# Kernel optimization log

Measured on AMD Instinct MI355X. Metric: run time of the kernel, lower is better.

Reference implementation:

```python
import jax, jax.numpy as jnp
import numpy as np

D_MODEL = 1024
N_HEADS = 16
D_K = D_MODEL // N_HEADS


def setup_inputs() -> dict:
    key = jax.random.key(0)
    ks = jax.random.split(key, 7)
    s = 1.0 / np.sqrt(D_MODEL)
    return {
        "x": jax.random.normal(ks[0], (2, 2048, D_MODEL), dtype=jnp.float32),
        "w_q": jax.random.uniform(ks[1], (D_MODEL, D_MODEL), jnp.float32, -s, s),
        "w_k": jax.random.uniform(ks[2], (D_MODEL, D_MODEL), jnp.float32, -s, s),
        "w_v": jax.random.uniform(ks[3], (D_MODEL, D_MODEL), jnp.float32, -s, s),
        "w_o": jax.random.uniform(ks[4], (D_MODEL, D_MODEL), jnp.float32, -s, s),
        "b_o": jax.random.uniform(ks[5], (D_MODEL,), jnp.float32, -s, s),
        "ln_gamma": jnp.ones((D_MODEL,), jnp.float32),
        "ln_beta": jnp.zeros((D_MODEL,), jnp.float32),
    }


def reference(x, w_q, w_k, w_v, w_o, b_o, ln_gamma, ln_beta):
    # Pre-LN
    mu = jnp.mean(x, axis=-1, keepdims=True)
    var = jnp.mean(jnp.square(x - mu), axis=-1, keepdims=True)
    x_norm = (x - mu) / jnp.sqrt(var + 1e-5) * ln_gamma + ln_beta

    B, S, _ = x.shape
    # torch Linear: y = x @ W.T ; weights stored [out, in]
    def proj(w):
        return (x_norm @ w.T).reshape(B, S, N_HEADS, D_K).transpose(0, 2, 1, 3)

    Q, K, V = proj(w_q), proj(w_k), proj(w_v)  # [B,H,S,Dk]
    scores = jnp.einsum("bhqd,bhkd->bhqk", Q, K) / np.sqrt(D_K)
    attn = jax.nn.softmax(scores, axis=-1)
    attended = jnp.einsum("bhqk,bhkd->bhqd", attn, V)
    attended = attended.transpose(0, 2, 1, 3).reshape(B, S, D_MODEL)
    out = attended @ w_o.T + b_o
    return x + out
```

## Files before the change

### kernel.cpp

```cpp
#include <hip/hip_runtime.h>

typedef _Float16 f16;
typedef _Float16 f16x8 __attribute__((ext_vector_type(8)));
typedef _Float16 f16x4 __attribute__((ext_vector_type(4)));
typedef float f32x4 __attribute__((ext_vector_type(4)));

#define SEQ   2048
#define DM    1024
#define DKH   64
#define MTOT  4096

__device__ __forceinline__ f32x4 mfma16(f16x8 a, f16x8 b, f32x4 c) {
  return __builtin_amdgcn_mfma_f32_16x16x32_f16(a, b, c, 0, 0, 0);
}

__device__ __forceinline__ void gload16(const f16* g, f16* l) {
  __builtin_amdgcn_global_load_lds(
      (const __attribute__((address_space(1))) void*)g,
      (__attribute__((address_space(3))) void*)l, 16, 0, 0);
}

__global__ __launch_bounds__(256) void cast_all(const float* __restrict__ w_q,
                                                const float* __restrict__ w_k,
                                                const float* __restrict__ w_v,
                                                const float* __restrict__ w_o,
                                                f16* __restrict__ out) {
  const int sel = blockIdx.x >> 10;
  const float* src = sel == 0 ? w_q : sel == 1 ? w_k : sel == 2 ? w_v : w_o;
  const int i = ((blockIdx.x & 1023) * 256 + threadIdx.x) * 4;
  float4 v = *reinterpret_cast<const float4*>(src + i);
  f16x4 o;
  o[0] = (f16)v.x; o[1] = (f16)v.y; o[2] = (f16)v.z; o[3] = (f16)v.w;
  *reinterpret_cast<f16x4*>(out + (size_t)sel * 1048576 + i) = o;
}

__global__ __launch_bounds__(256) void ln_kernel(const float* __restrict__ x,
                                                 const float* __restrict__ gamma,
                                                 const float* __restrict__ beta,
                                                 f16* __restrict__ xn) {
  const int row = blockIdx.x, t = threadIdx.x;
  const float* xr = x + (size_t)row * DM;
  float v[4], s = 0.f, s2 = 0.f;
#pragma unroll
  for (int i = 0; i < 4; ++i) {
    v[i] = xr[t + i * 256];
    s += v[i];
    s2 += v[i] * v[i];
  }
#pragma unroll
  for (int o = 32; o > 0; o >>= 1) {
    s  += __shfl_down(s, o);
    s2 += __shfl_down(s2, o);
  }
  __shared__ float ps[4], ps2[4], mu_s, rs_s;
  if ((t & 63) == 0) { ps[t >> 6] = s; ps2[t >> 6] = s2; }
  __syncthreads();
  if (t == 0) {
    float a = ps[0] + ps[1] + ps[2] + ps[3];
    float b = ps2[0] + ps2[1] + ps2[2] + ps2[3];
    float mu = a * (1.f / DM);
    float var = b * (1.f / DM) - mu * mu;
    mu_s = mu;
    rs_s = rsqrtf(var + 1e-5f);
  }
  __syncthreads();
  const float mu = mu_s, rs = rs_s;
#pragma unroll
  for (int i = 0; i < 4; ++i) {
    int d = t + i * 256;
    xn[(size_t)row * DM + d] = (f16)(((v[i] - mu) * rs) * gamma[d] + beta[d]);
  }
}

__global__ __launch_bounds__(256) void gemm_qkv(const f16* __restrict__ A,
                                                const f16* __restrict__ Wqkv,
                                                f16* __restrict__ qb,
                                                f16* __restrict__ kb,
                                                f16* __restrict__ vtb) {
  __shared__ f16 sA[128][64];
  __shared__ f16 sB[64][64];
  const int t = threadIdx.x, l = t & 63, w = t >> 6;
  const int wr = w >> 1, wc = w & 1, lg = l >> 4, lm = l & 15;
  const int m0 = blockIdx.y * 128, n0 = blockIdx.x * 64;
  const int crow = l >> 3;
  const int scol = ((l & 7) ^ crow) << 3;
  const int rsw  = (lm & 7) << 3;

  f32x4 acc[4][2] = {};

  for (int k0 = 0; k0 < DM; k0 += 64) {
    __syncthreads();
#pragma unroll
    for (int cc = 0; cc < 4; ++cc) {
      const int c = w + cc * 4;
      gload16(A + (size_t)(m0 + c * 8 + crow) * DM + k0 + scol, &sA[c * 8][0]);
    }
#pragma unroll
    for (int cc = 0; cc < 2; ++cc) {
      const int c = w + cc * 4;
      gload16(Wqkv + (size_t)(n0 + c * 8 + crow) * DM + k0 + scol, &sB[c * 8][0]);
    }
    __syncthreads();
#pragma unroll
    for (int kk = 0; kk < 2; ++kk) {
      f16x8 af[4], bf[2];
#pragma unroll
      for (int i = 0; i < 4; ++i)
        af[i] = *(const f16x8*)&sA[wr * 64 + i * 16 + lm][(kk * 32 + lg * 8) ^ rsw];
#pragma unroll
      for (int i = 0; i < 2; ++i)
        bf[i] = *(const f16x8*)&sB[wc * 32 + i * 16 + lm][(kk * 32 + lg * 8) ^ rsw];
#pragma unroll
      for (int mi = 0; mi < 4; ++mi)
#pragma unroll
        for (int ni = 0; ni < 2; ++ni)
          acc[mi][ni] = mfma16(af[mi], bf[ni], acc[mi][ni]);
    }
  }

  const int sel = blockIdx.x >> 4;
  if (sel < 2) {
    f16* outp = sel == 0 ? qb : kb;
    const int nloc = n0 - sel * 1024;
#pragma unroll
    for (int mi = 0; mi < 4; ++mi) {
      const int rowb = m0 + wr * 64 + mi * 16 + lg * 4;
#pragma unroll
      for (int ni = 0; ni < 2; ++ni) {
        const int col = nloc + wc * 32 + ni * 16 + lm;
#pragma unroll
        for (int r = 0; r < 4; ++r)
          outp[(size_t)(rowb + r) * DM + col] = (f16)acc[mi][ni][r];
      }
    }
  } else {
#pragma unroll
    for (int mi = 0; mi < 4; ++mi) {
      const int rowb = m0 + wr * 64 + mi * 16 + lg * 4;
      const int b = rowb >> 11, s = rowb & 2047;
#pragma unroll
      for (int ni = 0; ni < 2; ++ni) {
        const int col = (n0 - 2048) + wc * 32 + ni * 16 + lm;
        f16x4 o;
        o[0] = (f16)acc[mi][ni][0]; o[1] = (f16)acc[mi][ni][1];
        o[2] = (f16)acc[mi][ni][2]; o[3] = (f16)acc[mi][ni][3];
        *reinterpret_cast<f16x4*>(&vtb[(size_t)(b * 1024 + col) * SEQ + s]) = o;
      }
    }
  }
}

__global__ __launch_bounds__(256) void gemm_out(const f16* __restrict__ A,
                                                const f16* __restrict__ W,
                                                float* __restrict__ out,
                                                const float* __restrict__ bias,
                                                const float* __restrict__ resid) {
  __shared__ f16 sA[64][64];
  __shared__ f16 sB[128][64];
  const int t = threadIdx.x, l = t & 63, w = t >> 6;
  const int wr = w >> 1, wc = w & 1, lg = l >> 4, lm = l & 15;
  const int m0 = blockIdx.y * 64, n0 = blockIdx.x * 128;
  const int crow = l >> 3;
  const int scol = ((l & 7) ^ crow) << 3;
  const int rsw  = (lm & 7) << 3;

  f32x4 acc[2][4] = {};

  for (int k0 = 0; k0 < DM; k0 += 64) {
    __syncthreads();
#pragma unroll
    for (int cc = 0; cc < 2; ++cc) {
      const int c = w + cc * 4;
      gload16(A + (size_t)(m0 + c * 8 + crow) * DM + k0 + scol, &sA[c * 8][0]);
    }
#pragma unroll
    for (int cc = 0; cc < 4; ++cc) {
      const int c = w + cc * 4;
      gload16(W + (size_t)(n0 + c * 8 + crow) * DM + k0 + scol, &sB[c * 8][0]);
    }
    __syncthreads();
#pragma unroll
    for (int kk = 0; kk < 2; ++kk) {
      f16x8 af[2], bf[4];
#pragma unroll
      for (int i = 0; i < 2; ++i)
        af[i] = *(const f16x8*)&sA[wr * 32 + i * 16 + lm][(kk * 32 + lg * 8) ^ rsw];
#pragma unroll
      for (int i = 0; i < 4; ++i)
        bf[i] = *(const f16x8*)&sB[wc * 64 + i * 16 + lm][(kk * 32 + lg * 8) ^ rsw];
#pragma unroll
      for (int mi = 0; mi < 2; ++mi)
#pragma unroll
        for (int ni = 0; ni < 4; ++ni)
          acc[mi][ni] = mfma16(af[mi], bf[ni], acc[mi][ni]);
    }
  }

#pragma unroll
  for (int mi = 0; mi < 2; ++mi) {
    const int rowb = m0 + wr * 32 + mi * 16 + lg * 4;
#pragma unroll
    for (int ni = 0; ni < 4; ++ni) {
      const int col = n0 + wc * 64 + ni * 16 + lm;
#pragma unroll
      for (int r = 0; r < 4; ++r) {
        const size_t idx = (size_t)(rowb + r) * DM + col;
        out[idx] = resid[idx] + bias[col] + acc[mi][ni][r];
      }
    }
  }
}

__global__ __launch_bounds__(256) void attn_kernel(const f16* __restrict__ Qb,
                                                   const f16* __restrict__ Kb,
                                                   const f16* __restrict__ Vt,
                                                   f16* __restrict__ Ob) {
  __shared__ f16 sK[2][64][64];
  __shared__ f16 sV[2][64][64];

  int bx = blockIdx.x;
  bx = (bx & 7) * 128 + (bx >> 3);
  const int qt = bx & 31, bh = bx >> 5;
  const int h = bh & 15, b = bh >> 4;
  const int t = threadIdx.x, l = t & 63, w = t >> 6;
  const int lg = l >> 4, lm = l & 15;
  const float K2 = 0.18033688f;

  const f16* qptr = Qb + (size_t)(b * SEQ + qt * 64 + w * 16 + lm) * DM + h * DKH;
  f16x8 qf[2];
  qf[0] = *(const f16x8*)(qptr + lg * 8);
  qf[1] = *(const f16x8*)(qptr + 32 + lg * 8);
#pragma unroll
  for (int j = 0; j < 8; ++j) {
    qf[0][j] = (f16)((float)qf[0][j] * K2);
    qf[1][j] = (f16)((float)qf[1][j] * K2);
  }

  float lsum = 0.f;
  f32x4 oacc[4] = {};

  const int crow = l >> 3;
  const int scol = ((l & 7) ^ crow) << 3;
  const int rsw  = (lm & 7) << 3;

  auto stage = [&](int buf, int kt) {
#pragma unroll
    for (int cc = 0; cc < 2; ++cc) {
      const int c = w + cc * 4;
      const int row = c * 8 + crow;
      const int nfp = row >> 4, lgp = (row >> 2) & 3, rp = row & 3;
      const int key = (nfp >> 1) * 32 + lgp * 8 + (nfp & 1) * 4 + rp;
      gload16(Kb + (size_t)(b * SEQ + kt * 64 + key) * DM + h * DKH + scol,
              &sK[buf][c * 8][0]);
      gload16(Vt + (size_t)(bh * DKH + row) * SEQ + kt * 64 + scol,
              &sV[buf][c * 8][0]);
    }
  };

  stage(0, 0);
  __syncthreads();
  int cur = 0;

  for (int kt = 0; kt < SEQ / 64; ++kt) {
    if (kt < SEQ / 64 - 1) stage(cur ^ 1, kt + 1);

    f32x4 sc[4] = {};
    __builtin_amdgcn_s_setprio(1);
#pragma unroll
    for (int kk = 0; kk < 2; ++kk)
#pragma unroll
      for (int nf = 0; nf < 4; ++nf) {
        f16x8 kf = *(const f16x8*)&sK[cur][nf * 16 + lm][(kk * 32 + lg * 8) ^ rsw];
        sc[nf] = mfma16(kf, qf[kk], sc[nf]);
      }
    __builtin_amdgcn_s_setprio(0);

    f16x8 pf[2];
#pragma unroll
    for (int nf = 0; nf < 4; ++nf)
#pragma unroll
      for (int r = 0; r < 4; ++r) {
        float p = __builtin_amdgcn_exp2f(sc[nf][r]);
        lsum += p;
        pf[nf >> 1][(nf & 1) * 4 + r] = (f16)p;
      }

    __builtin_amdgcn_s_setprio(1);
#pragma unroll
    for (int ks = 0; ks < 2; ++ks)
#pragma unroll
      for (int ni = 0; ni < 4; ++ni) {
        f16x8 vf = *(const f16x8*)&sV[cur][ni * 16 + lm][(ks * 32 + lg * 8) ^ rsw];
        oacc[ni] = mfma16(pf[ks], vf, oacc[ni]);
      }
    __builtin_amdgcn_s_setprio(0);

    __syncthreads();
    cur ^= 1;
  }

  float denom = lsum;
  denom += __shfl_xor(denom, 16);
  denom += __shfl_xor(denom, 32);
  float rd[4];
#pragma unroll
  for (int r = 0; r < 4; ++r) rd[r] = 1.f / __shfl(denom, lg * 4 + r);

#pragma unroll
  for (int ni = 0; ni < 4; ++ni)
#pragma unroll
    for (int r = 0; r < 4; ++r) {
      const int q = qt * 64 + w * 16 + lg * 4 + r;
      const int d = ni * 16 + lm;
      Ob[(size_t)(b * SEQ + q) * DM + h * DKH + d] = (f16)(oacc[ni][r] * rd[r]);
    }
}

extern "C" void kernel_launch(void* const* d_in, const int* in_sizes, int n_in,
                              void* d_out, int out_size, void* d_ws, size_t ws_size,
                              hipStream_t stream) {
  const float* x   = (const float*)d_in[0];
  const float* w_q = (const float*)d_in[1];
  const float* w_k = (const float*)d_in[2];
  const float* w_v = (const float*)d_in[3];
  const float* w_o = (const float*)d_in[4];
  const float* b_o = (const float*)d_in[5];
  const float* lng = (const float*)d_in[6];
  const float* lnb = (const float*)d_in[7];
  float* out = (float*)d_out;

  char* ws = (char*)d_ws;
  const size_t MB = 1ull << 20;
  f16* xn   = (f16*)(ws + 0 * MB);
  f16* wqkv = (f16*)(ws + 8 * MB);
  f16* woh  = (f16*)(ws + 14 * MB);
  f16* qb   = (f16*)(ws + 16 * MB);
  f16* kb   = (f16*)(ws + 24 * MB);
  f16* vtb  = (f16*)(ws + 32 * MB);
  f16* att  = (f16*)(ws + 40 * MB);

  cast_all<<<4096, 256, 0, stream>>>(w_q, w_k, w_v, w_o, wqkv);
  ln_kernel<<<MTOT, 256, 0, stream>>>(x, lng, lnb, xn);

  gemm_qkv<<<dim3(48, 32), 256, 0, stream>>>(xn, wqkv, qb, kb, vtb);
  attn_kernel<<<1024, 256, 0, stream>>>(qb, kb, vtb, att);
  gemm_out<<<dim3(8, 64), 256, 0, stream>>>(att, woh, out, b_o, x);
}
```

Baseline: 127.7 us.

## Double query rows per attention block and compute denominators via MFMA

Each attention workgroup now handles 128 query rows (32 per wave) instead of 64, so every K/V tile staged into LDS is reused by twice as many MFMAs and half as many blocks are launched. The softmax denominator is now accumulated with an extra MFMA against a ones vector instead of scalar adds plus cross-lane shuffles, and probabilities are packed with cvt_pkrtz. The costs are higher register pressure, fewer blocks (512) to fill the GPU, and round-toward-zero fp16 conversion of the probabilities.

Measured after the change: 121.3 us. 5.0% less time.

```diff
diff --git a/kernel.cpp b/kernel.cpp
--- a/kernel.cpp
+++ b/kernel.cpp
@@ -3,6 +3,8 @@
 typedef _Float16 f16;
 typedef _Float16 f16x8 __attribute__((ext_vector_type(8)));
 typedef _Float16 f16x4 __attribute__((ext_vector_type(4)));
+typedef _Float16 f16x2 __attribute__((ext_vector_type(2)));
+typedef __fp16 fp16x2 __attribute__((ext_vector_type(2)));
 typedef float f32x4 __attribute__((ext_vector_type(4)));
 
 #define SEQ   2048
@@ -12,6 +14,11 @@
 
 __device__ __forceinline__ f32x4 mfma16(f16x8 a, f16x8 b, f32x4 c) {
   return __builtin_amdgcn_mfma_f32_16x16x32_f16(a, b, c, 0, 0, 0);
+}
+
+__device__ __forceinline__ f16x2 cvt_pk(float a, float b) {
+  fp16x2 r = __builtin_amdgcn_cvt_pkrtz(a, b);
+  return __builtin_bit_cast(f16x2, r);
 }
 
 __device__ __forceinline__ void gload16(const f16* g, f16* l) {
@@ -219,25 +226,32 @@
   __shared__ f16 sV[2][64][64];
 
   int bx = blockIdx.x;
-  bx = (bx & 7) * 128 + (bx >> 3);
-  const int qt = bx & 31, bh = bx >> 5;
+  bx = (bx & 7) * 64 + (bx >> 3);
+  const int qt = bx & 15, bh = bx >> 4;
   const int h = bh & 15, b = bh >> 4;
   const int t = threadIdx.x, l = t & 63, w = t >> 6;
   const int lg = l >> 4, lm = l & 15;
   const float K2 = 0.18033688f;
 
-  const f16* qptr = Qb + (size_t)(b * SEQ + qt * 64 + w * 16 + lm) * DM + h * DKH;
-  f16x8 qf[2];
-  qf[0] = *(const f16x8*)(qptr + lg * 8);
-  qf[1] = *(const f16x8*)(qptr + 32 + lg * 8);
-#pragma unroll
-  for (int j = 0; j < 8; ++j) {
-    qf[0][j] = (f16)((float)qf[0][j] * K2);
-    qf[1][j] = (f16)((float)qf[1][j] * K2);
-  }
-
-  float lsum = 0.f;
-  f32x4 oacc[4] = {};
+  f16x8 qf[2][2];
+#pragma unroll
+  for (int qg = 0; qg < 2; ++qg) {
+    const f16* qptr =
+        Qb + (size_t)(b * SEQ + qt * 128 + w * 32 + qg * 16 + lm) * DM + h * DKH;
+    qf[qg][0] = *(const f16x8*)(qptr + lg * 8);
+    qf[qg][1] = *(const f16x8*)(qptr + 32 + lg * 8);
+#pragma unroll
+    for (int j = 0; j < 8; ++j) {
+      qf[qg][0][j] = (f16)((float)qf[qg][0][j] * K2);
+      qf[qg][1][j] = (f16)((float)qf[qg][1][j] * K2);
+    }
+  }
+
+  const f16x8 ones = {(f16)1, (f16)1, (f16)1, (f16)1,
+                      (f16)1, (f16)1, (f16)1, (f16)1};
+
+  f32x4 oacc[2][4] = {};
+  f32x4 oden[2] = {};
 
   const int crow = l >> 3;
   const int scol = ((l & 7) ^ crow) << 3;
@@ -264,56 +278,64 @@
   for (int kt = 0; kt < SEQ / 64; ++kt) {
     if (kt < SEQ / 64 - 1) stage(cur ^ 1, kt + 1);
 
-    f32x4 sc[4] = {};
+    f32x4 sc[2][4] = {};
     __builtin_amdgcn_s_setprio(1);
 #pragma unroll
     for (int kk = 0; kk < 2; ++kk)
 #pragma unroll
       for (int nf = 0; nf < 4; ++nf) {
         f16x8 kf = *(const f16x8*)&sK[cur][nf * 16 + lm][(kk * 32 + lg * 8) ^ rsw];
-        sc[nf] = mfma16(kf, qf[kk], sc[nf]);
+        sc[0][nf] = mfma16(kf, qf[0][kk], sc[0][nf]);
+        sc[1][nf] = mfma16(kf, qf[1][kk], sc[1][nf]);
       }
     __builtin_amdgcn_s_setprio(0);
 
-    f16x8 pf[2];
-#pragma unroll
-    for (int nf = 0; nf < 4; ++nf)
-#pragma unroll
-      for (int r = 0; r < 4; ++r) {
-        float p = __builtin_amdgcn_exp2f(sc[nf][r]);
-        lsum += p;
-        pf[nf >> 1][(nf & 1) * 4 + r] = (f16)p;
+    union PU { f16x8 v; f16x2 h[4]; };
+    PU pu[2][2];
+#pragma unroll
+    for (int qg = 0; qg < 2; ++qg)
+#pragma unroll
+      for (int nf = 0; nf < 4; ++nf) {
+        float e0 = __builtin_amdgcn_exp2f(sc[qg][nf][0]);
+        float e1 = __builtin_amdgcn_exp2f(sc[qg][nf][1]);
+        float e2 = __builtin_amdgcn_exp2f(sc[qg][nf][2]);
+        float e3 = __builtin_amdgcn_exp2f(sc[qg][nf][3]);
+        pu[qg][nf >> 1].h[(nf & 1) * 2 + 0] = cvt_pk(e0, e1);
+        pu[qg][nf >> 1].h[(nf & 1) * 2 + 1] = cvt_pk(e2, e3);
       }
 
     __builtin_amdgcn_s_setprio(1);
 #pragma unroll
-    for (int ks = 0; ks < 2; ++ks)
+    for (int ks = 0; ks < 2; ++ks) {
 #pragma unroll
       for (int ni = 0; ni < 4; ++ni) {
         f16x8 vf = *(const f16x8*)&sV[cur][ni * 16 + lm][(ks * 32 + lg * 8) ^ rsw];
-        oacc[ni] = mfma16(pf[ks], vf, oacc[ni]);
-      }
+        oacc[0][ni] = mfma16(pu[0][ks].v, vf, oacc[0][ni]);
+        oacc[1][ni] = mfma16(pu[1][ks].v, vf, oacc[1][ni]);
+      }
+      oden[0] = mfma16(pu[0][ks].v, ones, oden[0]);
+      oden[1] = mfma16(pu[1][ks].v, ones, oden[1]);
+    }
     __builtin_amdgcn_s_setprio(0);
 
     __syncthreads();
     cur ^= 1;
   }
 
-  float denom = lsum;
-  denom += __shfl_xor(denom, 16);
-  denom += __shfl_xor(denom, 32);
-  float rd[4];
-#pragma unroll
-  for (int r = 0; r < 4; ++r) rd[r] = 1.f / __shfl(denom, lg * 4 + r);
-
-#pragma unroll
-  for (int ni = 0; ni < 4; ++ni)
-#pragma unroll
-    for (int r = 0; r < 4; ++r) {
-      const int q = qt * 64 + w * 16 + lg * 4 + r;
-      const int d = ni * 16 + lm;
-      Ob[(size_t)(b * SEQ + q) * DM + h * DKH + d] = (f16)(oacc[ni][r] * rd[r]);
-    }
+#pragma unroll
+  for (int qg = 0; qg < 2; ++qg) {
+    float rd[4];
+#pragma unroll
+    for (int r = 0; r < 4; ++r) rd[r] = 1.f / oden[qg][r];
+#pragma unroll
+    for (int ni = 0; ni < 4; ++ni)
+#pragma unroll
+      for (int r = 0; r < 4; ++r) {
+        const int q = qt * 128 + w * 32 + qg * 16 + lg * 4 + r;
+        const int d = ni * 16 + lm;
+        Ob[(size_t)(b * SEQ + q) * DM + h * DKH + d] = (f16)(oacc[qg][ni][r] * rd[r]);
+      }
+  }
 }
 
 extern "C" void kernel_launch(void* const* d_in, const int* in_sizes, int n_in,
@@ -343,6 +365,6 @@
   ln_kernel<<<MTOT, 256, 0, stream>>>(x, lng, lnb, xn);
 
   gemm_qkv<<<dim3(48, 32), 256, 0, stream>>>(xn, wqkv, qb, kb, vtb);
-  attn_kernel<<<1024, 256, 0, stream>>>(qb, kb, vtb, att);
+  attn_kernel<<<512, 256, 0, stream>>>(qb, kb, vtb, att);
   gemm_out<<<dim3(8, 64), 256, 0, stream>>>(att, woh, out, b_o, x);
 }
```
